# Kernel optimization log

Measured on AMD Instinct MI355X. Metric: run time of the kernel, lower is better.

The kernel has to match this reference:

```python
import jax, jax.numpy as jnp
import numpy as np
from jax import lax

N_ITERS = 3
NUM_CAPS_IN = 768   # 32 * 4 * 6
NUM_CAPS_OUT = 64
CAPS_DIM_IN = 8
CAPS_DIM_OUT = 16


def _conv2d(x, w, b, stride):
    # x: NCHW, w: OIHW, VALID padding
    y = lax.conv_general_dilated(x, w, (stride, stride), 'VALID',
                                 dimension_numbers=('NCHW', 'OIHW', 'NCHW'))
    return y + b[None, :, None, None]


def _squash(x, axis):
    # norm**2 / (1 + norm**2) * x / norm  (as in the torch source)
    norm = jnp.linalg.norm(x, axis=axis, keepdims=True)
    return (norm ** 2) / (1.0 + norm ** 2) * x / norm


def setup_inputs() -> dict:
    key = jax.random.key(0)
    ks = jax.random.split(key, 4)
    B = 128
    x = jax.random.normal(ks[0], (B, 3, 32, 42), dtype=jnp.float32)
    conv1_w = jax.random.normal(ks[1], (32, 3, 6, 6), dtype=jnp.float32) * 0.1
    conv1_b = jnp.zeros((32,), dtype=jnp.float32)
    pc_w = jax.random.normal(ks[2], (256, 32, 3, 3), dtype=jnp.float32) * 0.1
    pc_b = jnp.zeros((256,), dtype=jnp.float32)
    # FinalCapsule W: (num_caps_in, num_caps_out, caps_dim_out, caps_dim_in)
    route_w = jax.random.normal(ks[3], (NUM_CAPS_IN, NUM_CAPS_OUT, CAPS_DIM_OUT, CAPS_DIM_IN), dtype=jnp.float32)
    return {"x": x, "conv1_w": conv1_w, "conv1_b": conv1_b,
            "pc_w": pc_w, "pc_b": pc_b, "route_w": route_w}


def reference(x, conv1_w, conv1_b, pc_w, pc_b, route_w):
    B = x.shape[0]
    # conv1: k=6, s=3 -> (B,32,9,13)
    h = jax.nn.relu(_conv2d(x, conv1_w, conv1_b, 3))
    # primary capsules: k=3, s=2 -> (B,256,4,6) -> (B,768,8)
    h = _conv2d(h, pc_w, pc_b, 2)
    u = h.reshape(B, -1, CAPS_DIM_IN)
    u = _squash(u, axis=-1)
    # prediction vectors: W[i,o,:,:] @ u[b,i,:] -> xh (B, 768, 64, 16)
    xh = jnp.einsum('iokd,bid->biok', route_w, u)
    xhd = lax.stop_gradient(xh)
    b_logits = jnp.zeros((B, NUM_CAPS_IN, NUM_CAPS_OUT), dtype=xh.dtype)
    for _ in range(N_ITERS - 1):
        c = jax.nn.softmax(b_logits, axis=2)                      # (B,768,64)
        s = jnp.sum(c[..., None] * xhd, axis=1, keepdims=True)   # (B,1,64,16)
        v = _squash(s, axis=-1)
        b_logits = b_logits + jnp.sum(xhd * v, axis=-1)
    c = jax.nn.softmax(b_logits, axis=2)
    s = jnp.sum(c[..., None] * xh, axis=1, keepdims=True)
    v = _squash(s, axis=-1)                                       # (B,1,64,16)
    return v[:, 0].reshape(B, NUM_CAPS_OUT * CAPS_DIM_OUT)        # (B,1024)
```

## Files before the change

### kernel.cpp

```cpp
#include <hip/hip_runtime.h>
#include <math.h>

typedef __attribute__((ext_vector_type(8))) short bfrag;
typedef __attribute__((ext_vector_type(4))) float f32x4;
typedef __attribute__((ext_vector_type(16))) float f32x16;
typedef __attribute__((ext_vector_type(4))) unsigned short ushort4v;
typedef unsigned short u16;

__device__ __forceinline__ float b2f(u16 h) { return __uint_as_float((unsigned)h << 16); }
__device__ __forceinline__ u16 f2b(float x) { return (u16)(__float_as_uint(x) >> 16); }

__device__ __forceinline__ void split8(const float* x, bfrag& hi, bfrag& lo) {
    #pragma unroll
    for (int j = 0; j < 8; ++j) {
        unsigned xb = __float_as_uint(x[j]);
        unsigned hb = xb & 0xffff0000u;
        float lf = x[j] - __uint_as_float(hb);
        hi[j] = (short)(xb >> 16);
        lo[j] = (short)(__float_as_uint(lf) >> 16);
    }
}
__device__ __forceinline__ void trunc8(const float* x, bfrag& hi) {
    #pragma unroll
    for (int j = 0; j < 8; ++j) hi[j] = (short)(__float_as_uint(x[j]) >> 16);
}

__global__ __launch_bounds__(256) void front_kernel(
    const float* __restrict__ x, const float* __restrict__ w1,
    const float* __restrict__ b1, float* __restrict__ B2) {
    __shared__ float xl[4032];
    __shared__ float wl[3456];
    __shared__ float hl[3744];
    int b = blockIdx.x, tid = threadIdx.x;
    const float* xb = x + (size_t)b * 4032;
    #pragma unroll
    for (int i = 0; i < 4; ++i) {
        int idx = tid + 256 * i;
        if (idx < 1008) *(float4*)(xl + idx * 4) = *(const float4*)(xb + idx * 4);
        if (idx < 864)  *(float4*)(wl + idx * 4) = *(const float4*)(w1 + idx * 4);
    }
    __syncthreads();
    for (int idx = tid; idx < 3744; idx += 256) {
        int oc = idx / 117, r = idx % 117;
        int oh = r / 13, ow = r % 13;
        float acc = b1[oc];
        #pragma unroll
        for (int ic = 0; ic < 3; ++ic) {
            const float* xc = xl + ic * 1344 + (oh * 3) * 42 + ow * 3;
            const float* wc = wl + (oc * 3 + ic) * 36;
            #pragma unroll
            for (int kh = 0; kh < 6; ++kh)
                #pragma unroll
                for (int kw = 0; kw < 6; ++kw)
                    acc += xc[kh * 42 + kw] * wc[kh * 6 + kw];
        }
        hl[idx] = fmaxf(acc, 0.f);
    }
    __syncthreads();
    for (int f = tid; f < 864; f += 256) {
        int ko = f / 24, s = f % 24;
        int h = s / 6, w = s % 6;
        float o8[8];
        #pragma unroll
        for (int j = 0; j < 8; ++j) {
            int k = ko * 8 + j;
            int ic = k / 9, rr = k % 9;
            int kh = rr / 3, kw = rr % 3;
            o8[j] = hl[ic * 117 + (2 * h + kh) * 13 + (2 * w + kw)];
        }
        float* dst = B2 + ((size_t)ko * 3072 + b * 24 + s) * 8;
        *(float4*)dst = *(const float4*)o8;
        *(float4*)(dst + 4) = *(const float4*)(o8 + 4);
    }
}

__global__ __launch_bounds__(256) void pc_gemm_kernel(
    const float* __restrict__ wpc, const float* __restrict__ bias,
    const float* __restrict__ B2, float* __restrict__ u2) {
    int wv = threadIdx.x >> 6;
    int l = threadIdx.x & 63;
    int q = l >> 4, r16 = l & 15;
    int c2t = blockIdx.y * 4 + wv;
    int n0 = blockIdx.x * 16;
    f32x4 acc = {0.f, 0.f, 0.f, 0.f};
    const float* ap0 = wpc + (size_t)(c2t * 16 + r16) * 288 + q * 8;
    const float* bp0 = B2 + ((size_t)q * 3072 + n0 + r16) * 8;
    #pragma unroll
    for (int ks = 0; ks < 9; ++ks) {
        float av[8], bv[8];
        *(float4*)av = *(const float4*)(ap0 + ks * 32);
        *(float4*)(av + 4) = *(const float4*)(ap0 + ks * 32 + 4);
        *(float4*)bv = *(const float4*)(bp0 + (size_t)ks * 98304);
        *(float4*)(bv + 4) = *(const float4*)(bp0 + (size_t)ks * 98304 + 4);
        bfrag ahi, alo, bhi, blo;
        split8(av, ahi, alo);
        split8(bv, bhi, blo);
        acc = __builtin_amdgcn_mfma_f32_16x16x32_bf16(ahi, bhi, acc, 0, 0, 0);
        acc = __builtin_amdgcn_mfma_f32_16x16x32_bf16(ahi, blo, acc, 0, 0, 0);
        acc = __builtin_amdgcn_mfma_f32_16x16x32_bf16(alo, bhi, acc, 0, 0, 0);
    }
    int n = n0 + r16;
    int b = n / 24, s = n % 24;
    float vals[4], n2[4];
    #pragma unroll
    for (int r = 0; r < 4; ++r) {
        float xv = acc[r] + bias[c2t * 16 + q * 4 + r];
        vals[r] = xv;
        n2[r] = xv * xv;
    }
    #pragma unroll
    for (int r = 0; r < 4; ++r) {
        n2[r] += __shfl_xor(n2[r], 1, 64);
        n2[r] += __shfl_xor(n2[r], 2, 64);
        n2[r] += __shfl_xor(n2[r], 4, 64);
    }
    #pragma unroll
    for (int r = 0; r < 4; ++r) {
        int c2 = c2t * 16 + q * 4 + r;
        int cap = c2 * 3 + (s >> 3);
        int d = s & 7;
        float nr = sqrtf(n2[r]);
        u2[((size_t)(cap * 2 + (d >> 2)) * 128 + b) * 4 + (d & 3)]
            = vals[r] * nr / (1.f + n2[r]);
    }
}

__global__ __launch_bounds__(256) void zsum_kernel(
    const u16* __restrict__ blogb, float* __restrict__ zsum) {
    int i = blockIdx.x;
    int tid = threadIdx.x;
    int b = tid >> 1, oh = tid & 1;
    const u16* src = blogb + (size_t)oh * 32 * 98304 + (size_t)i * 128 + b;
    float sum = 0.f;
    #pragma unroll
    for (int o = 0; o < 32; ++o) sum += __expf(b2f(src[(size_t)o * 98304]));
    sum += __shfl_xor(sum, 1, 64);
    if (!oh) zsum[i * 128 + b] = sum;
}

template <bool UNIFORM>
__global__ __launch_bounds__(256, 4) void spass_kernel(
    const float* __restrict__ W, const float* __restrict__ u2,
    const u16* __restrict__ blogb, const float* __restrict__ zsum,
    u16* __restrict__ s_part) {
    int o = blockIdx.x;
    int it = blockIdx.y;
    int tid = threadIdx.x;
    int wv = tid >> 6;
    int l = tid & 63;
    int q = l >> 4, r16 = l & 15;
    int i0 = it * 64;
    __shared__ unsigned short whi[64 * 136];
    __shared__ unsigned short wlo[64 * 136];

    float4 ua[3][2][2];
    float blv[3][2], zv[3][2];
    auto issue = [&](int s, int buf) {
        int cap = i0 + s * 4 + q;
        #pragma unroll
        for (int m = 0; m < 2; ++m) {
            int b = wv * 32 + m * 16 + r16;
            ua[buf][m][0] = *(const float4*)(u2 + ((size_t)(cap * 2 + 0) * 128 + b) * 4);
            ua[buf][m][1] = *(const float4*)(u2 + ((size_t)(cap * 2 + 1) * 128 + b) * 4);
            if (!UNIFORM) {
                blv[buf][m] = b2f(blogb[((size_t)o * 768 + cap) * 128 + b]);
                zv[buf][m]  = zsum[cap * 128 + b];
            }
        }
    };

    issue(0, 0);
    issue(1, 1);
    #pragma unroll
    for (int itr = 0; itr < 8; ++itr) {
        int F = tid + 256 * itr;
        int cap = F >> 5, slot = F & 31;
        float4 t4 = *(const float4*)(W + ((size_t)(i0 + cap) * 64 + o) * 128 + slot * 4);
        ushort4v h4, l4;
        float tf[4] = {t4.x, t4.y, t4.z, t4.w};
        #pragma unroll
        for (int j = 0; j < 4; ++j) {
            unsigned xb = __float_as_uint(tf[j]);
            float lf = tf[j] - __uint_as_float(xb & 0xffff0000u);
            h4[j] = (unsigned short)(xb >> 16);
            l4[j] = (unsigned short)(__float_as_uint(lf) >> 16);
        }
        *(ushort4v*)(whi + cap * 136 + slot * 4) = h4;
        *(ushort4v*)(wlo + cap * 136 + slot * 4) = l4;
    }
    __syncthreads();

    f32x4 acc0 = {0.f, 0.f, 0.f, 0.f};
    f32x4 acc1 = {0.f, 0.f, 0.f, 0.f};
    #pragma unroll
    for (int s = 0; s < 16; ++s) {
        int cur = s % 3;
        if (s < 14) issue(s + 2, (s + 2) % 3);
        int wrow = (s * 4 + q) * 136 + r16 * 8;
        bfrag bhi = *(const bfrag*)(whi + wrow);
        bfrag blo = *(const bfrag*)(wlo + wrow);
        #pragma unroll
        for (int m = 0; m < 2; ++m) {
            float uv[8];
            *(float4*)(uv) = ua[cur][m][0];
            *(float4*)(uv + 4) = ua[cur][m][1];
            if (!UNIFORM) {
                float c = __expf(blv[cur][m]) / zv[cur][m];
                #pragma unroll
                for (int j = 0; j < 8; ++j) uv[j] *= c;
            }
            bfrag ahi;
            trunc8(uv, ahi);
            if (m == 0) {
                acc0 = __builtin_amdgcn_mfma_f32_16x16x32_bf16(ahi, bhi, acc0, 0, 0, 0);
                acc0 = __builtin_amdgcn_mfma_f32_16x16x32_bf16(ahi, blo, acc0, 0, 0, 0);
            } else {
                acc1 = __builtin_amdgcn_mfma_f32_16x16x32_bf16(ahi, bhi, acc1, 0, 0, 0);
                acc1 = __builtin_amdgcn_mfma_f32_16x16x32_bf16(ahi, blo, acc1, 0, 0, 0);
            }
        }
    }
    #pragma unroll
    for (int reg = 0; reg < 4; ++reg) {
        int b0 = wv * 32 + q * 4 + reg;
        s_part[(((size_t)it * 128 + b0) * 64 + o) * 16 + r16] = f2b(acc0[reg]);
        s_part[(((size_t)it * 128 + b0 + 16) * 64 + o) * 16 + r16] = f2b(acc1[reg]);
    }
}

template <bool TRANSPOSED>
__global__ __launch_bounds__(256) void squashv_kernel(
    const u16* __restrict__ s_part, float* __restrict__ v, float scale) {
    int idx = blockIdx.x * 256 + threadIdx.x;
    float acc = 0.f;
    #pragma unroll
    for (int it = 0; it < 12; ++it) acc += b2f(s_part[(size_t)it * 131072 + idx]);
    acc *= scale;
    float n2 = acc * acc;
    n2 += __shfl_xor(n2, 1, 64);
    n2 += __shfl_xor(n2, 2, 64);
    n2 += __shfl_xor(n2, 4, 64);
    n2 += __shfl_xor(n2, 8, 64);
    float n = sqrtf(n2);
    float val = acc * n / (1.f + n2);
    if (TRANSPOSED) {
        int k = idx & 15, o = (idx >> 4) & 63, b = idx >> 10;
        v[((size_t)o * 128 + b) * 16 + k] = val;
    } else {
        v[idx] = val;
    }
}

template <bool ACCUM>
__global__ __launch_bounds__(256, 4) void bpass_kernel(
    const float* __restrict__ W, const float* __restrict__ u2,
    const float* __restrict__ v_t, u16* __restrict__ blogb) {
    int o = blockIdx.x, it = blockIdx.y;
    int tid = threadIdx.x;
    int wv = tid >> 6;
    int l = tid & 63;
    int r = l & 31;
    int kh = l >> 5;
    int capB = it * 32;
    __shared__ float wl[32 * 164];
    #pragma unroll
    for (int itr = 0; itr < 4; ++itr) {
        int F = tid + 256 * itr;
        int cap = F >> 5, slot = F & 31;
        int k = slot >> 1, dh = slot & 1;
        float4 t4 = *(const float4*)(W + ((size_t)(capB + cap) * 64 + o) * 128 + k * 8 + dh * 4);
        float* dst = wl + cap * 164 + (dh * 4) * 20 + k;
        dst[0] = t4.x; dst[20] = t4.y; dst[40] = t4.z; dst[60] = t4.w;
    }
    bfrag vt[4];
    #pragma unroll
    for (int nt = 0; nt < 4; ++nt) {
        const float* vp = v_t + ((size_t)o * 128 + nt * 32 + r) * 16 + kh * 8;
        float vv8[8];
        *(float4*)(vv8) = *(const float4*)vp;
        *(float4*)(vv8 + 4) = *(const float4*)(vp + 4);
        trunc8(vv8, vt[nt]);
    }
    __syncthreads();
    #pragma unroll
    for (int mt = 0; mt < 2; ++mt) {
        int cl = wv * 8 + mt * 4 + (r >> 3);
        const float* ap = wl + cl * 164 + (r & 7) * 20 + kh * 8;
        float a8[8];
        *(float4*)(a8) = *(const float4*)ap;
        *(float4*)(a8 + 4) = *(const float4*)(ap + 4);
        int capg = capB + wv * 8 + mt * 4;
        int gw = kh * 2;
        float prevv[4][2];
        if (ACCUM) {
            #pragma unroll
            for (int nt = 0; nt < 4; ++nt) {
                int b = nt * 32 + r;
                #pragma unroll
                for (int gg = 0; gg < 2; ++gg)
                    prevv[nt][gg] = b2f(blogb[((size_t)o * 768 + capg + gw + gg) * 128 + b]);
            }
        }
        float4 u4b[2][4];
        #pragma unroll
        for (int g = 0; g < 4; ++g)
            u4b[0][g] = *(const float4*)(u2 + ((size_t)((capg + g) * 2 + kh) * 128 + r) * 4);
        bfrag ahi, alo;
        split8(a8, ahi, alo);
        #pragma unroll
        for (int nt = 0; nt < 4; ++nt) {
            int cur = nt & 1;
            if (nt < 3) {
                int bn = (nt + 1) * 32 + r;
                #pragma unroll
                for (int g = 0; g < 4; ++g)
                    u4b[cur ^ 1][g] = *(const float4*)(u2 + ((size_t)((capg + g) * 2 + kh) * 128 + bn) * 4);
            }
            int b = nt * 32 + r;
            f32x16 acc;
            #pragma unroll
            for (int z = 0; z < 16; ++z) acc[z] = 0.f;
            acc = __builtin_amdgcn_mfma_f32_32x32x16_bf16(ahi, vt[nt], acc, 0, 0, 0);
            acc = __builtin_amdgcn_mfma_f32_32x32x16_bf16(alo, vt[nt], acc, 0, 0, 0);
            float full[4];
            #pragma unroll
            for (int g = 0; g < 4; ++g) {
                float part = u4b[cur][g].x * acc[g * 4 + 0] + u4b[cur][g].y * acc[g * 4 + 1]
                           + u4b[cur][g].z * acc[g * 4 + 2] + u4b[cur][g].w * acc[g * 4 + 3];
                full[g] = part + __shfl_xor(part, 32, 64);
            }
            #pragma unroll
            for (int gg = 0; gg < 2; ++gg) {
                int g = gw + gg;
                size_t bi = ((size_t)o * 768 + capg + g) * 128 + b;
                blogb[bi] = f2b((ACCUM ? prevv[nt][gg] : 0.f) + full[g]);
            }
        }
    }
}

extern "C" void kernel_launch(void* const* d_in, const int* in_sizes, int n_in,
                              void* d_out, int out_size, void* d_ws, size_t ws_size,
                              hipStream_t stream) {
    const float* x  = (const float*)d_in[0];
    const float* w1 = (const float*)d_in[1];
    const float* b1 = (const float*)d_in[2];
    const float* wp = (const float*)d_in[3];
    const float* bp = (const float*)d_in[4];
    const float* W  = (const float*)d_in[5];
    float* out = (float*)d_out;
    float* ws = (float*)d_ws;

    float* u2     = ws;
    u16*   blogb  = (u16*)(ws + 786432);
    float* zsum   = ws + 3932160;
    float* v      = ws + 4030464;
    u16*   s_part = (u16*)(ws + 4161536);
    float* B2     = ws + 4947968;

    front_kernel<<<128, 256, 0, stream>>>(x, w1, b1, B2);
    pc_gemm_kernel<<<dim3(192, 4), 256, 0, stream>>>(wp, bp, B2, u2);

    spass_kernel<true><<<dim3(64, 12), 256, 0, stream>>>(W, u2, nullptr, nullptr, s_part);
    squashv_kernel<true><<<512, 256, 0, stream>>>(s_part, v, 1.f / 64.f);
    bpass_kernel<false><<<dim3(64, 24), 256, 0, stream>>>(W, u2, v, blogb);

    zsum_kernel<<<768, 256, 0, stream>>>(blogb, zsum);
    spass_kernel<false><<<dim3(64, 12), 256, 0, stream>>>(W, u2, blogb, zsum, s_part);
    squashv_kernel<true><<<512, 256, 0, stream>>>(s_part, v, 1.f);
    bpass_kernel<true><<<dim3(64, 24), 256, 0, stream>>>(W, u2, v, blogb);

    zsum_kernel<<<768, 256, 0, stream>>>(blogb, zsum);
    spass_kernel<false><<<dim3(64, 12), 256, 0, stream>>>(W, u2, blogb, zsum, s_part);
    squashv_kernel<false><<<512, 256, 0, stream>>>(s_part, out, 1.f);
}
```

Measured before the change: 136.1 us.

## Fuse squash reduction into spass via last-block atomic counter

Removes the separate squashv kernel launches. Each spass block increments a per-output-capsule counter after writing its partial sums, and the last of the 12 blocks for that capsule reduces the partials and applies the squash. Counters are reset in front_kernel and bpass. This drops three launches and their serialization gaps. In exchange it adds fences and atomics, and the final reduction runs on only 64 blocks, which may serialize work at the tail.

```diff
diff --git a/kernel.cpp b/kernel.cpp
--- a/kernel.cpp
+++ b/kernel.cpp
@@ -27,11 +27,12 @@
 
 __global__ __launch_bounds__(256) void front_kernel(
     const float* __restrict__ x, const float* __restrict__ w1,
-    const float* __restrict__ b1, float* __restrict__ B2) {
+    const float* __restrict__ b1, float* __restrict__ B2, int* __restrict__ done) {
     __shared__ float xl[4032];
     __shared__ float wl[3456];
     __shared__ float hl[3744];
     int b = blockIdx.x, tid = threadIdx.x;
+    if (b == 0 && tid < 64) done[tid] = 0;
     const float* xb = x + (size_t)b * 4032;
     #pragma unroll
     for (int i = 0; i < 4; ++i) {
@@ -138,11 +139,12 @@
     if (!oh) zsum[i * 128 + b] = sum;
 }
 
-template <bool UNIFORM>
+template <bool UNIFORM, bool FINAL>
 __global__ __launch_bounds__(256, 4) void spass_kernel(
     const float* __restrict__ W, const float* __restrict__ u2,
     const u16* __restrict__ blogb, const float* __restrict__ zsum,
-    u16* __restrict__ s_part) {
+    u16* __restrict__ s_part, float* __restrict__ vout,
+    int* __restrict__ done, float scale) {
     int o = blockIdx.x;
     int it = blockIdx.y;
     int tid = threadIdx.x;
@@ -152,6 +154,7 @@
     int i0 = it * 64;
     __shared__ unsigned short whi[64 * 136];
     __shared__ unsigned short wlo[64 * 136];
+    __shared__ int winner;
 
     float4 ua[3][2][2];
     float blv[3][2], zv[3][2];
@@ -226,37 +229,51 @@
         s_part[(((size_t)it * 128 + b0) * 64 + o) * 16 + r16] = f2b(acc0[reg]);
         s_part[(((size_t)it * 128 + b0 + 16) * 64 + o) * 16 + r16] = f2b(acc1[reg]);
     }
-}
-
-template <bool TRANSPOSED>
-__global__ __launch_bounds__(256) void squashv_kernel(
-    const u16* __restrict__ s_part, float* __restrict__ v, float scale) {
-    int idx = blockIdx.x * 256 + threadIdx.x;
-    float acc = 0.f;
-    #pragma unroll
-    for (int it = 0; it < 12; ++it) acc += b2f(s_part[(size_t)it * 131072 + idx]);
-    acc *= scale;
-    float n2 = acc * acc;
-    n2 += __shfl_xor(n2, 1, 64);
-    n2 += __shfl_xor(n2, 2, 64);
-    n2 += __shfl_xor(n2, 4, 64);
-    n2 += __shfl_xor(n2, 8, 64);
-    float n = sqrtf(n2);
-    float val = acc * n / (1.f + n2);
-    if (TRANSPOSED) {
-        int k = idx & 15, o = (idx >> 4) & 63, b = idx >> 10;
-        v[((size_t)o * 128 + b) * 16 + k] = val;
+
+    __threadfence();
+    __syncthreads();
+    if (tid == 0) {
+        int old = __hip_atomic_fetch_add(done + o, 1, __ATOMIC_ACQ_REL,
+                                         __HIP_MEMORY_SCOPE_AGENT);
+        winner = (old == 11);
+    }
+    __syncthreads();
+    if (!winner) return;
+    __threadfence();
+    int b = tid >> 1, kh = tid & 1;
+    const u16* sp = s_part + ((size_t)b * 64 + o) * 16 + kh * 8;
+    float a8[8] = {0.f, 0.f, 0.f, 0.f, 0.f, 0.f, 0.f, 0.f};
+    #pragma unroll
+    for (int it2 = 0; it2 < 12; ++it2) {
+        const u16* p = sp + (size_t)it2 * 131072;
+        #pragma unroll
+        for (int j = 0; j < 8; ++j) a8[j] += b2f(p[j]);
+    }
+    float n2p = 0.f;
+    #pragma unroll
+    for (int j = 0; j < 8; ++j) { a8[j] *= scale; n2p += a8[j] * a8[j]; }
+    float n2 = n2p + __shfl_xor(n2p, 1, 64);
+    float nr = sqrtf(n2);
+    float sc = nr / (1.f + n2);
+    if (FINAL) {
+        float* dst = vout + (size_t)b * 1024 + o * 16 + kh * 8;
+        #pragma unroll
+        for (int j = 0; j < 8; ++j) dst[j] = a8[j] * sc;
     } else {
-        v[idx] = val;
+        float* dst = vout + ((size_t)o * 128 + b) * 16 + kh * 8;
+        #pragma unroll
+        for (int j = 0; j < 8; ++j) dst[j] = a8[j] * sc;
     }
 }
 
 template <bool ACCUM>
 __global__ __launch_bounds__(256, 4) void bpass_kernel(
     const float* __restrict__ W, const float* __restrict__ u2,
-    const float* __restrict__ v_t, u16* __restrict__ blogb) {
+    const float* __restrict__ v_t, u16* __restrict__ blogb,
+    int* __restrict__ done) {
     int o = blockIdx.x, it = blockIdx.y;
     int tid = threadIdx.x;
+    if (it == 0 && tid == 0) done[o] = 0;
     int wv = tid >> 6;
     int l = tid & 63;
     int r = l & 31;
@@ -357,20 +374,21 @@
     float* v      = ws + 4030464;
     u16*   s_part = (u16*)(ws + 4161536);
     float* B2     = ws + 4947968;
-
-    front_kernel<<<128, 256, 0, stream>>>(x, w1, b1, B2);
+    int*   done   = (int*)(ws + 5832704);
+
+    front_kernel<<<128, 256, 0, stream>>>(x, w1, b1, B2, done);
     pc_gemm_kernel<<<dim3(192, 4), 256, 0, stream>>>(wp, bp, B2, u2);
 
-    spass_kernel<true><<<dim3(64, 12), 256, 0, stream>>>(W, u2, nullptr, nullptr, s_part);
-    squashv_kernel<true><<<512, 256, 0, stream>>>(s_part, v, 1.f / 64.f);
-    bpass_kernel<false><<<dim3(64, 24), 256, 0, stream>>>(W, u2, v, blogb);
+    spass_kernel<true, false><<<dim3(64, 12), 256, 0, stream>>>(
+        W, u2, nullptr, nullptr, s_part, v, done, 1.f / 64.f);
+    bpass_kernel<false><<<dim3(64, 24), 256, 0, stream>>>(W, u2, v, blogb, done);
 
     zsum_kernel<<<768, 256, 0, stream>>>(blogb, zsum);
-    spass_kernel<false><<<dim3(64, 12), 256, 0, stream>>>(W, u2, blogb, zsum, s_part);
-    squashv_kernel<true><<<512, 256, 0, stream>>>(s_part, v, 1.f);
-    bpass_kernel<true><<<dim3(64, 24), 256, 0, stream>>>(W, u2, v, blogb);
+    spass_kernel<false, false><<<dim3(64, 12), 256, 0, stream>>>(
+        W, u2, blogb, zsum, s_part, v, done, 1.f);
+    bpass_kernel<true><<<dim3(64, 24), 256, 0, stream>>>(W, u2, v, blogb, done);
 
     zsum_kernel<<<768, 256, 0, stream>>>(blogb, zsum);
-    spass_kernel<false><<<dim3(64, 12), 256, 0, stream>>>(W, u2, blogb, zsum, s_part);
-    squashv_kernel<false><<<512, 256, 0, stream>>>(s_part, out, 1.f);
-}
+    spass_kernel<false, true><<<dim3(64, 12), 256, 0, stream>>>(
+        W, u2, blogb, zsum, s_part, out, done, 1.f);
+}
```

Result: slower. 457.1 us (+235.8%).
